# Kernel tuning notes

Hardware: AMD Instinct MI355X
Metric: run time of the kernel (lower is better)

The kernel has to match this reference:

```python
import jax, jax.numpy as jnp
import numpy as np
from functools import partial

U, I, D, E = 8192, 8192, 128, 524288
N = U + I


def setup_inputs() -> dict:
    key = jax.random.key(0)
    ks = jax.random.split(key, 12)
    s = 1.0 / np.sqrt(D)
    return {
        "user_emb": jax.random.normal(ks[0], (U, D), jnp.float32) * 0.1,
        "item_emb": jax.random.normal(ks[1], (I, D), jnp.float32) * 0.1,
        "adj_rows": jax.random.randint(ks[2], (E,), 0, N, jnp.int32),
        "adj_cols": jax.random.randint(ks[3], (E,), 0, N, jnp.int32),
        "adj_vals": jax.random.uniform(ks[4], (E,), jnp.float32) * (1.0 / 32.0),
        "wq": jax.random.normal(ks[5], (D, D), jnp.float32) * s,
        "bq": jnp.zeros((D,), jnp.float32),
        "wk": jax.random.normal(ks[6], (D, D), jnp.float32) * s,
        "bk": jnp.zeros((D,), jnp.float32),
        "wv": jax.random.normal(ks[7], (D, D), jnp.float32) * s,
        "bv": jnp.zeros((D,), jnp.float32),
        "fw": jax.random.normal(ks[8], (D, D), jnp.float32) * s,
        "fb": jnp.zeros((D,), jnp.float32),
        "n_layers": 3,
        "topk": 32,
    }


def _spmm(vals, rows, cols, x):
    # sparse [N,N] @ dense [N,D] via gather + segment_sum
    return jax.ops.segment_sum(vals[:, None] * x[cols], rows, num_segments=N)


def reference(user_emb, item_emb, adj_rows, adj_cols, adj_vals,
              wq, bq, wk, bk, wv, bv, fw, fb, n_layers, topk):
    ego = jnp.concatenate([user_emb, item_emb], axis=0)  # [N, D]
    layers = []
    for _ in range(n_layers):
        ego = _spmm(adj_vals, adj_rows, adj_cols, ego)
        layers.append(ego)
    all_emb = jnp.mean(jnp.stack(layers, axis=1), axis=1)  # [N, D]

    # full similarity + topk + gather
    sim = ego @ ego.T                                # [N, N]
    idx = jax.lax.top_k(sim, topk)[1]                # [N, K]
    samples = jnp.take(ego, idx, axis=0)             # [N, K, D]

    # per-node small attention over the K samples (dropout = eval identity)
    q = ego @ wq.T + bq                              # [N, D]
    k_ = samples @ wk.T + bk                         # [N, K, D]
    v = samples @ wv.T + bv                          # [N, K, D]
    scores = jnp.einsum('nd,nkd->nk', q, k_) / jnp.sqrt(jnp.float32(D))
    attn = jax.nn.softmax(scores, axis=-1)
    atten_embed = jnp.einsum('nk,nkd->nd', attn, v) + 0.1 * ego

    # fusion gating (softmax over dim=1, i.e. the node axis, as in source)
    a1 = jnp.tanh(all_emb @ fw.T + fb)
    a2 = jnp.tanh(atten_embed @ fw.T + fb)
    a = jax.nn.softmax(jnp.stack([a1, a2], axis=0), axis=1)  # [2, N, D]
    fusion = a[0] * all_emb + a[1] * atten_embed

    return (all_emb[:U], all_emb[U:],
            atten_embed[:U], atten_embed[U:],
            fusion[:U], fusion[U:])
```

## Files before the change

kernel.cpp:

```cpp
#include <hip/hip_runtime.h>
#include <math.h>

#define U_ 8192
#define I_ 8192
#define D_ 128
#define E_ 524288
#define N_ 16384
#define K_ 32
#define CAP_ 512

typedef unsigned short u16;
typedef unsigned int u32;
typedef unsigned long long u64;
typedef __attribute__((ext_vector_type(8))) short bf16x8;
typedef __attribute__((ext_vector_type(4))) float f32x4;

__global__ void k_init(const float* __restrict__ wq, const float* __restrict__ wk,
                       const float* __restrict__ bq, const float* __restrict__ wv,
                       const float* __restrict__ fw,
                       float* __restrict__ M, float* __restrict__ bqk,
                       float* __restrict__ wvT, float* __restrict__ fwdT,
                       int* __restrict__ cnt, float* __restrict__ cs1,
                       float* __restrict__ cs2,
                       float* __restrict__ svec, int* __restrict__ gcount,
                       int* __restrict__ failn) {
  const int tid = blockIdx.x * 256 + threadIdx.x;
  cnt[tid] = 0;
  gcount[tid] = 0;
  if (tid < 2048) { cs1[tid] = 0.f; cs2[tid] = 0.f; }
  if (tid < 128) svec[tid] = 0.f;
  if (tid == 0) *failn = 0;
  const int i = tid >> 7, j = tid & 127;
  float s = 0.f;
  for (int l = 0; l < 128; ++l) s += wq[l * 128 + i] * wk[l * 128 + j];
  M[tid] = s;
  wvT[i * 128 + j] = wv[j * 128 + i];
  fwdT[i * 128 + j] = fw[j * 128 + i];
  if (tid < 128) {
    float s2 = 0.f;
    for (int l = 0; l < 128; ++l) s2 += bq[l] * wk[l * 128 + tid];
    bqk[tid] = s2;
  }
}

__global__ void k_concat(const float* __restrict__ user, const float* __restrict__ item,
                         float* __restrict__ ego,
                         const int* __restrict__ rows, int* __restrict__ cnt) {
  const int i = blockIdx.x * 256 + threadIdx.x;
  const float4 v = (i < U_ * D_ / 4) ? ((const float4*)user)[i]
                                     : ((const float4*)item)[i - U_ * D_ / 4];
  ((float4*)ego)[i] = v;
  atomicAdd(&cnt[rows[i]], 1);
}

__global__ void k_scan(const int* __restrict__ cnt, int* __restrict__ row_ptr,
                       int* __restrict__ cursor) {
  __shared__ int wsum[16];
  __shared__ int carry_s;
  const int t = threadIdx.x;
  const int lane = t & 63, wid = t >> 6;
  if (t == 0) carry_s = 0;
  __syncthreads();
  for (int c = 0; c < N_ / 1024; ++c) {
    const int x = cnt[c * 1024 + t];
    int incl = x;
#pragma unroll
    for (int off = 1; off < 64; off <<= 1) {
      const int v = __shfl_up(incl, off, 64);
      if (lane >= off) incl += v;
    }
    if (lane == 63) wsum[wid] = incl;
    __syncthreads();
    if (wid == 0) {
      int s = (lane < 16) ? wsum[lane] : 0;
#pragma unroll
      for (int off = 1; off < 16; off <<= 1) {
        const int v = __shfl_up(s, off, 64);
        if (lane >= off) s += v;
      }
      if (lane < 16) wsum[lane] = s;
    }
    __syncthreads();
    const int carry = carry_s;
    const int wbase = wid ? wsum[wid - 1] : 0;
    const int excl = carry + wbase + incl - x;
    row_ptr[c * 1024 + t] = excl;
    cursor[c * 1024 + t] = excl;
    __syncthreads();
    if (t == 1023) carry_s += wsum[15];
    __syncthreads();
  }
  if (t == 0) row_ptr[N_] = carry_s;
}

__global__ void k_scatter(const int* __restrict__ rows, const int* __restrict__ cols,
                          const float* __restrict__ vals, int* __restrict__ cursor,
                          int* __restrict__ ccol, float* __restrict__ cval) {
  const int e = blockIdx.x * 256 + threadIdx.x;
  const int r = rows[e];
  const int p = atomicAdd(&cursor[r], 1);
  ccol[p] = cols[e];
  cval[p] = vals[e];
}

__global__ __launch_bounds__(128) void k_spmm(const float* __restrict__ x,
                                              float* __restrict__ y,
                                              float* __restrict__ sum,
                                              const int* __restrict__ row_ptr,
                                              const int* __restrict__ ccol,
                                              const float* __restrict__ cval,
                                              const int first, const int last) {
  const int r = blockIdx.x, d = threadIdx.x;
  const int b = row_ptr[r], e = row_ptr[r + 1];
  double a[8];
#pragma unroll
  for (int u = 0; u < 8; ++u) a[u] = 0.0;
  int i = b;
  for (; i < e && (i & 3); ++i)
    a[0] += (double)cval[i] * (double)x[ccol[i] * 128 + d];
  for (; i + 7 < e; i += 8) {
    const int4 ca = *(const int4*)&ccol[i];
    const int4 cb = *(const int4*)&ccol[i + 4];
    const float4 va = *(const float4*)&cval[i];
    const float4 vb = *(const float4*)&cval[i + 4];
    a[0] += (double)va.x * (double)x[ca.x * 128 + d];
    a[1] += (double)va.y * (double)x[ca.y * 128 + d];
    a[2] += (double)va.z * (double)x[ca.z * 128 + d];
    a[3] += (double)va.w * (double)x[ca.w * 128 + d];
    a[4] += (double)vb.x * (double)x[cb.x * 128 + d];
    a[5] += (double)vb.y * (double)x[cb.y * 128 + d];
    a[6] += (double)vb.z * (double)x[cb.z * 128 + d];
    a[7] += (double)vb.w * (double)x[cb.w * 128 + d];
  }
  for (; i < e; ++i)
    a[0] += (double)cval[i] * (double)x[ccol[i] * 128 + d];
  const float f = (float)((((a[0] + a[1]) + (a[2] + a[3])) + ((a[4] + a[5]) + (a[6] + a[7]))));
  y[r * 128 + d] = f;
  float s = first ? f : sum[r * 128 + d] + f;
  if (last) s = s / 3.0f;
  sum[r * 128 + d] = s;
}

__global__ __launch_bounds__(256) void k_split_t(const float* __restrict__ x,
                                                 u16* __restrict__ Gh, u16* __restrict__ Gl,
                                                 u16* __restrict__ XTh, u16* __restrict__ XTl,
                                                 float* __restrict__ svec) {
  __shared__ u16 lh[128 * 66];
  __shared__ u16 ll[128 * 66];
  const int tid = threadIdx.x;
  const int r0 = blockIdx.x * 64;
  float colsum = 0.f;
  for (int s = 0; s < 32; ++s) {
    const int idx = tid + s * 256;
    const int r = idx >> 7, d = idx & 127;
    const float v = x[(r0 + r) * 128 + d];
    colsum += v;
    unsigned int u = __float_as_uint(v);
    u += 0x7fffu + ((u >> 16) & 1u);
    const u16 h = (u16)(u >> 16);
    const float hf = __uint_as_float(((unsigned int)h) << 16);
    const float l = v - hf;
    unsigned int u2 = __float_as_uint(l);
    u2 += 0x7fffu + ((u2 >> 16) & 1u);
    const u16 lo = (u16)(u2 >> 16);
    Gh[(r0 + r) * 128 + d] = h;
    Gl[(r0 + r) * 128 + d] = lo;
    lh[d * 66 + r] = h;
    ll[d * 66 + r] = lo;
  }
  atomicAdd(&svec[tid & 127], colsum);
  __syncthreads();
  for (int s = 0; s < 32; ++s) {
    const int idx = tid + s * 256;
    const int d = idx >> 6, rr = idx & 63;
    XTh[d * 16384 + r0 + rr] = lh[d * 66 + rr];
    XTl[d * 16384 + r0 + rr] = ll[d * 66 + rr];
  }
}

__global__ __launch_bounds__(256) void k_c2mfma(const u16* __restrict__ XTh,
                                                const u16* __restrict__ XTl,
                                                float* __restrict__ C2part) {
  const int tid = threadIdx.x, w = tid >> 6, lane = tid & 63;
  const int n16 = lane & 15, kq = lane >> 4;
  const int c0 = blockIdx.x * 64;
  f32x4 acc[2][8];
#pragma unroll
  for (int a = 0; a < 2; ++a)
#pragma unroll
    for (int b = 0; b < 8; ++b) acc[a][b] = (f32x4){0.f, 0.f, 0.f, 0.f};
  for (int ks = 0; ks < 2; ++ks) {
    const int c = c0 + ks * 32 + kq * 8;
    bf16x8 Fh[8], Fl[8];
#pragma unroll
    for (int g = 0; g < 8; ++g) {
      const int base = (g * 16 + n16) * 16384 + c;
      Fh[g] = *(const bf16x8*)&XTh[base];
      Fl[g] = *(const bf16x8*)&XTl[base];
    }
#pragma unroll
    for (int a = 0; a < 2; ++a) {
      const int tr = w * 2 + a;
#pragma unroll
      for (int b = 0; b < 8; ++b) {
        acc[a][b] = __builtin_amdgcn_mfma_f32_16x16x32_bf16(Fl[tr], Fh[b], acc[a][b], 0, 0, 0);
        acc[a][b] = __builtin_amdgcn_mfma_f32_16x16x32_bf16(Fh[tr], Fl[b], acc[a][b], 0, 0, 0);
        acc[a][b] = __builtin_amdgcn_mfma_f32_16x16x32_bf16(Fh[tr], Fh[b], acc[a][b], 0, 0, 0);
      }
    }
  }
  float* dst = C2part + (size_t)blockIdx.x * 16384;
#pragma unroll
  for (int a = 0; a < 2; ++a) {
    const int tr = w * 2 + a;
#pragma unroll
    for (int b = 0; b < 8; ++b)
#pragma unroll
      for (int i = 0; i < 4; ++i)
        dst[(tr * 16 + kq * 4 + i) * 128 + b * 16 + n16] = acc[a][b][i];
  }
}

__global__ void k_c2red(const float* __restrict__ C2part, float* __restrict__ C2) {
  const int e = blockIdx.x * 256 + threadIdx.x;
  float s = 0.f;
  for (int b = 0; b < 256; ++b) s += C2part[(size_t)b * 16384 + e];
  C2[e] = s;
}

__global__ __launch_bounds__(128) void k_tau(const float* __restrict__ x,
                                             const float* __restrict__ C2,
                                             const float* __restrict__ svec,
                                             float* __restrict__ tau) {
  __shared__ float xs[8][128];
  __shared__ double r1[8][2], r2[8][2];
  const int tid = threadIdx.x;
  const int lane = tid & 63, wid = tid >> 6;
  const int n0 = blockIdx.x * 8;
#pragma unroll
  for (int rr = 0; rr < 8; ++rr) xs[rr][tid] = x[(n0 + rr) * 128 + tid];
  __syncthreads();
  double y[8];
#pragma unroll
  for (int rr = 0; rr < 8; ++rr) y[rr] = 0.0;
  for (int k2 = 0; k2 < 128; ++k2) {
    const double c = (double)C2[k2 * 128 + tid];
#pragma unroll
    for (int rr = 0; rr < 8; ++rr) y[rr] += (double)xs[rr][k2] * c;
  }
  const double sv = (double)svec[tid];
#pragma unroll
  for (int rr = 0; rr < 8; ++rr) {
    double v1 = (double)xs[rr][tid] * y[rr];
    double v2 = (double)xs[rr][tid] * sv;
#pragma unroll
    for (int off = 32; off; off >>= 1) {
      v1 += __shfl_xor(v1, off, 64);
      v2 += __shfl_xor(v2, off, 64);
    }
    if (lane == 0) { r1[rr][wid] = v1; r2[rr][wid] = v2; }
  }
  __syncthreads();
  if (tid < 8) {
    const double exy = (r1[tid][0] + r1[tid][1]) / 16384.0;
    const double m = (r2[tid][0] + r2[tid][1]) / 16384.0;
    double var = exy - m * m;
    if (var < 0.0) var = 0.0;
    tau[n0 + tid] = (float)(m + 2.55 * sqrt(var));
  }
}

__global__ __launch_bounds__(256) void k_qk(const float* __restrict__ ego,
                                            const float* __restrict__ M,
                                            const float* __restrict__ bqk,
                                            float* __restrict__ qkout) {
  __shared__ float xs[8][128];
  const int tid = threadIdx.x;
  const int r0 = blockIdx.x * 8;
#pragma unroll
  for (int s = 0; s < 4; ++s) {
    const int idx = tid + s * 256;
    xs[idx >> 7][idx & 127] = ego[r0 * 128 + idx];
  }
  __syncthreads();
  const int j = tid & 127, h = tid >> 7;
  const float bj = bqk[j];
  float acc[4];
#pragma unroll
  for (int r = 0; r < 4; ++r) acc[r] = bj;
  for (int d = 0; d < 128; d += 4) {
    const float w0 = M[(d + 0) * 128 + j];
    const float w1 = M[(d + 1) * 128 + j];
    const float w2 = M[(d + 2) * 128 + j];
    const float w3 = M[(d + 3) * 128 + j];
#pragma unroll
    for (int r = 0; r < 4; ++r) {
      const float4 xv = *(const float4*)&xs[h * 4 + r][d];
      acc[r] += xv.x * w0 + xv.y * w1 + xv.z * w2 + xv.w * w3;
    }
  }
#pragma unroll
  for (int r = 0; r < 4; ++r)
    qkout[(r0 + h * 4 + r) * 128 + j] = acc[r];
}

__device__ __forceinline__ void gload_lds16(const u16* g, u16* l) {
  __builtin_amdgcn_global_load_lds(
      (const __attribute__((address_space(1))) void*)g,
      (__attribute__((address_space(3))) void*)l, 16, 0, 0);
}

__global__ __launch_bounds__(256) void k_simmfma(const u16* __restrict__ Gh,
                                                 const u16* __restrict__ Gl,
                                                 const float* __restrict__ tau,
                                                 int* __restrict__ gstripcnt,
                                                 int2* __restrict__ gbuf) {
  __shared__ __align__(16) u16 lh[64 * 128];
  __shared__ int cnt128[128];
  const int tid = threadIdx.x;
  const int w = tid >> 6, lane = tid & 63;
  const int strip = blockIdx.x & 15, rgrp = blockIdx.x >> 4;
  const int n16 = lane & 15, kq = lane >> 4;

  if (tid < 128) cnt128[tid] = 0;

  const int rowbase = rgrp * 128 + w * 32;
  bf16x8 Bh[2][4], Bl[2][4];
#pragma unroll
  for (int rg = 0; rg < 2; ++rg) {
    const int row = rowbase + rg * 16 + n16;
#pragma unroll
    for (int q = 0; q < 4; ++q) {
      Bh[rg][q] = *(const bf16x8*)&Gh[row * 128 + q * 32 + kq * 8];
      Bl[rg][q] = *(const bf16x8*)&Gl[row * 128 + q * 32 + kq * 8];
    }
  }
  const float tau0 = tau[rowbase + n16];
  const float tau1 = tau[rowbase + 16 + n16];
  const int col0 = strip * 1024;

  for (int st = 0; st < 16; ++st) {
    const int cb = col0 + st * 64;
    __syncthreads();
#pragma unroll
    for (int ii = 0; ii < 4; ++ii) {
      const int srow = w * 16 + ii * 4 + kq;
      const int chunk = n16 ^ (srow & 7);
      gload_lds16(Gh + (((size_t)(cb + srow)) << 7) + chunk * 8,
                  lh + ((w * 16 + ii * 4) << 7));
    }
    __syncthreads();
#pragma unroll
    for (int ct = 0; ct < 4; ++ct) {
      const int ar = ct * 16 + n16;
      const char* lbase = (const char*)lh + ar * 256;
      bf16x8 Ah[4];
#pragma unroll
      for (int q = 0; q < 4; ++q)
        Ah[q] = *(const bf16x8*)(lbase + ((q * 64 + kq * 16) ^ ((ar & 7) << 4)));
#pragma unroll
      for (int rg = 0; rg < 2; ++rg) {
        f32x4 p = {0.f, 0.f, 0.f, 0.f};
        f32x4 r = {0.f, 0.f, 0.f, 0.f};
#pragma unroll
        for (int q = 0; q < 4; ++q) {
          p = __builtin_amdgcn_mfma_f32_16x16x32_bf16(Ah[q], Bh[rg][q], p, 0, 0, 0);
          r = __builtin_amdgcn_mfma_f32_16x16x32_bf16(Ah[q], Bl[rg][q], r, 0, 0, 0);
        }
        const float tv = rg ? tau1 : tau0;
        const int lrow = w * 32 + rg * 16 + n16;
        const int row = rgrp * 128 + lrow;
#pragma unroll
        for (int i = 0; i < 4; ++i) {
          const float v = p[i] + r[i];
          if (v > tv) {
            const int c = cb + ct * 16 + kq * 4 + i;
            const int pos = atomicAdd(&cnt128[lrow], 1);
            if (pos < 32)
              gbuf[row * CAP_ + strip * 32 + pos] = make_int2(c, __float_as_int(v));
          }
        }
      }
    }
  }
  __syncthreads();
  if (tid < 128) gstripcnt[(rgrp * 128 + tid) * 16 + strip] = cnt128[tid];
}

__global__ __launch_bounds__(256) void k_refine(const int* __restrict__ gstripcnt,
                                                const int2* __restrict__ gbuf,
                                                int* __restrict__ topk_idx,
                                                int* __restrict__ failq,
                                                int* __restrict__ failn) {
  __shared__ u64 lk[4][CAP_];
  const int tid = threadIdx.x, w = tid >> 6, lane = tid & 63;
  const int n = blockIdx.x * 4 + w;

  const int scn = (lane < 16) ? gstripcnt[n * 16 + lane] : 0;
  int total = 0, over = 0;
#pragma unroll
  for (int s = 0; s < 16; ++s) {
    const int c = __shfl(scn, s, 64);
    total += c;
    over |= (c > 32);
  }
  const int bad = (total < 36 || total > CAP_ || over);
  const int cnt = bad ? 0 : total;

  int base = 0;
#pragma unroll
  for (int s = 0; s < 16; ++s) {
    const int c = __shfl(scn, s, 64);
    if (!bad && lane < c) {
      const int2 p = gbuf[n * CAP_ + s * 32 + lane];
      u32 uv = (u32)p.y;
      uv = (uv >> 31) ? ~uv : (uv | 0x80000000u);
      lk[w][base + lane] = ((u64)uv << 32) | (u64)(16383 - p.x);
    }
    base += bad ? 0 : c;
  }
  __syncthreads();

  for (int ci = lane; ci < cnt; ci += 64) {
    const u64 kk = lk[w][ci];
    int r = 0;
#pragma unroll 4
    for (int j = 0; j < cnt; ++j)
      r += (lk[w][j] > kk) ? 1 : 0;
    if (r < 32) topk_idx[n * 32 + r] = 16383 - (int)(u32)(kk & 0xffffffffu);
  }
  if (bad) {
    if (lane == 0) {
      const int s = atomicAdd(failn, 1);
      if (s < 64) failq[s] = n;
    }
    if (lane < 32) topk_idx[n * 32 + lane] = 0;
  }
}

__global__ __launch_bounds__(256) void k_fallback(const float* __restrict__ x,
                                                  const int* __restrict__ failq,
                                                  const int* __restrict__ failn,
                                                  double* __restrict__ fsim,
                                                  int* __restrict__ topk_idx) {
  const int nf = *failn;
  const int which = blockIdx.x;
  if (which >= nf || which >= 64) return;
  const int row = failq[which];
  __shared__ float xs[128];
  __shared__ double bm[256];
  __shared__ int bc[256];
  const int tid = threadIdx.x;
  if (tid < 128) xs[tid] = x[row * 128 + tid];
  __syncthreads();
  double* fs = fsim + (size_t)which * 16384;
  for (int c = tid; c < 16384; c += 256) {
    const float4* xp = (const float4*)&x[c * 128];
    double a = 0.0;
    for (int d = 0; d < 32; ++d) {
      const float4 v = xp[d];
      a += (double)xs[d * 4 + 0] * (double)v.x + (double)xs[d * 4 + 1] * (double)v.y +
           (double)xs[d * 4 + 2] * (double)v.z + (double)xs[d * 4 + 3] * (double)v.w;
    }
    fs[c] = a;
  }
  __syncthreads();
  for (int r = 0; r < 32; ++r) {
    double m = -1.0e300; int mc = 0;
    for (int c = tid; c < 16384; c += 256) {
      const double v = fs[c];
      if (v > m || (v == m && c < mc)) { m = v; mc = c; }
    }
    bm[tid] = m; bc[tid] = mc;
    __syncthreads();
    for (int s = 128; s; s >>= 1) {
      if (tid < s) {
        if (bm[tid + s] > bm[tid] || (bm[tid + s] == bm[tid] && bc[tid + s] < bc[tid])) {
          bm[tid] = bm[tid + s]; bc[tid] = bc[tid + s];
        }
      }
      __syncthreads();
    }
    if (tid == 0) { topk_idx[row * 32 + r] = bc[0]; fs[bc[0]] = -1.0e300; }
    __syncthreads();
  }
}

__global__ __launch_bounds__(256) void k_attn(const float* __restrict__ ego,
                                              float* __restrict__ qk,
                                              const int* __restrict__ topk_idx) {
  __shared__ float qv[128];
  __shared__ float sm[32 * 130];
  __shared__ int tki[32];
  __shared__ float sc[32];
  __shared__ float psum[256];
  const int n = blockIdx.x, tid = threadIdx.x;
  if (tid < 128) qv[tid] = qk[n * 128 + tid];
  if (tid < 32) tki[tid] = topk_idx[n * 32 + tid] & 16383;
  __syncthreads();
  for (int e = tid; e < 2048; e += 256) {
    const int k2 = e >> 6, d2 = e & 63;
    const float2 v = *(const float2*)&ego[(size_t)tki[k2] * 128 + d2 * 2];
    *(float2*)&sm[k2 * 130 + d2 * 2] = v;
  }
  __syncthreads();
  {
    const int kk = tid & 31, part = tid >> 5;
    float s = 0.f;
    const int d0 = part * 16;
    for (int d = d0; d < d0 + 16; ++d) s += qv[d] * sm[kk * 130 + d];
    psum[tid] = s;
  }
  __syncthreads();
  if (tid < 32) {
    float v = 0.f;
#pragma unroll
    for (int p = 0; p < 8; ++p) v += psum[tid + p * 32];
    v *= (1.0f / 11.313708498984760f);
    float m = v;
#pragma unroll
    for (int off = 16; off; off >>= 1) m = fmaxf(m, __shfl_xor(m, off, 32));
    const float e = expf(v - m);
    float ssum = e;
#pragma unroll
    for (int off = 16; off; off >>= 1) ssum += __shfl_xor(ssum, off, 32);
    sc[tid] = e / ssum;
  }
  __syncthreads();
  {
    const int d = tid & 127, half = tid >> 7;
    float s = 0.f;
    const int k0 = half * 16;
    for (int k2 = k0; k2 < k0 + 16; ++k2) s += sc[k2] * sm[k2 * 130 + d];
    psum[tid] = s;
  }
  __syncthreads();
  if (tid < 128) qk[n * 128 + tid] = psum[tid] + psum[tid + 128];
}

__global__ __launch_bounds__(256) void k_attnfuse(const float* __restrict__ sa,
                                                  const float* __restrict__ ego,
                                                  const float* __restrict__ allemb,
                                                  const float* __restrict__ wvT,
                                                  const float* __restrict__ bv,
                                                  const float* __restrict__ fwdT,
                                                  const float* __restrict__ fb,
                                                  float* __restrict__ atten,
                                                  float* __restrict__ z1,
                                                  float* __restrict__ z2,
                                                  float* __restrict__ cs1,
                                                  float* __restrict__ cs2) {
  __shared__ float xs[8][128];
  __shared__ float xa[8][128];
  __shared__ float as_[8][128];
  __shared__ float red1[2][128];
  __shared__ float red2[2][128];
  const int tid = threadIdx.x;
  const int r0 = blockIdx.x * 8;
#pragma unroll
  for (int s = 0; s < 4; ++s) {
    const int idx = tid + s * 256;
    const int rr = idx >> 7, d = idx & 127;
    xs[rr][d] = sa[(r0 + rr) * 128 + d];
    xa[rr][d] = allemb[(r0 + rr) * 128 + d];
  }
  __syncthreads();
  const int j = tid & 127, h = tid >> 7;
  {
    const float bj = bv[j];
    float acc[4];
#pragma unroll
    for (int r = 0; r < 4; ++r) acc[r] = bj;
    for (int d = 0; d < 128; d += 4) {
      const float w0 = wvT[(d + 0) * 128 + j];
      const float w1 = wvT[(d + 1) * 128 + j];
      const float w2 = wvT[(d + 2) * 128 + j];
      const float w3 = wvT[(d + 3) * 128 + j];
#pragma unroll
      for (int r = 0; r < 4; ++r) {
        const float4 xv = *(const float4*)&xs[h * 4 + r][d];
        acc[r] += xv.x * w0 + xv.y * w1 + xv.z * w2 + xv.w * w3;
      }
    }
#pragma unroll
    for (int r = 0; r < 4; ++r) {
      const int n = r0 + h * 4 + r;
      const float av = acc[r] + 0.1f * ego[n * 128 + j];
      atten[n * 128 + j] = av;
      as_[h * 4 + r][j] = av;
    }
  }
  __syncthreads();
  const float fbj = fb[j];
  float acc1[4], acc2[4];
#pragma unroll
  for (int r = 0; r < 4; ++r) { acc1[r] = fbj; acc2[r] = fbj; }
  for (int d = 0; d < 128; d += 4) {
    const float w0 = fwdT[(d + 0) * 128 + j];
    const float w1 = fwdT[(d + 1) * 128 + j];
    const float w2 = fwdT[(d + 2) * 128 + j];
    const float w3 = fwdT[(d + 3) * 128 + j];
#pragma unroll
    for (int r = 0; r < 4; ++r) {
      const int rr = h * 4 + r;
      const float4 xv = *(const float4*)&xa[rr][d];
      const float4 av = *(const float4*)&as_[rr][d];
      acc1[r] += xv.x * w0 + xv.y * w1 + xv.z * w2 + xv.w * w3;
      acc2[r] += av.x * w0 + av.y * w1 + av.z * w2 + av.w * w3;
    }
  }
  float ls1 = 0.f, ls2 = 0.f;
#pragma unroll
  for (int r = 0; r < 4; ++r) {
    const int rr = h * 4 + r;
    const float t1 = tanhf(acc1[r]);
    const float t2 = tanhf(acc2[r]);
    z1[(r0 + rr) * 128 + j] = t1;
    z2[(r0 + rr) * 128 + j] = t2;
    ls1 += expf(t1 - 1.0f);
    ls2 += expf(t2 - 1.0f);
  }
  red1[h][j] = ls1;
  red2[h][j] = ls2;
  __syncthreads();
  if (h == 0) {
    const int rep = blockIdx.x & 15;
    atomicAdd(&cs1[rep * 128 + j], red1[0][j] + red1[1][j]);
    atomicAdd(&cs2[rep * 128 + j], red2[0][j] + red2[1][j]);
  }
}

__global__ void k_fuse2(const float* __restrict__ allemb, const float* __restrict__ atten,
                        const float* __restrict__ z1, const float* __restrict__ z2,
                        const float* __restrict__ cs1, const float* __restrict__ cs2,
                        float* __restrict__ fusion) {
  __shared__ float s1[128], s2[128];
  const int tid = threadIdx.x;
  if (tid < 128) {
    float a = 0.f, b = 0.f;
#pragma unroll
    for (int rep = 0; rep < 16; ++rep) {
      a += cs1[rep * 128 + tid];
      b += cs2[rep * 128 + tid];
    }
    s1[tid] = a; s2[tid] = b;
  }
  __syncthreads();
  const int i = blockIdx.x * 256 + tid;
  const int j0 = (i & 31) * 4;
  const float4 zv1 = ((const float4*)z1)[i];
  const float4 zv2 = ((const float4*)z2)[i];
  const float4 xv = ((const float4*)allemb)[i];
  const float4 av = ((const float4*)atten)[i];
  float4 o;
  o.x = expf(zv1.x - 1.0f) / s1[j0 + 0] * xv.x + expf(zv2.x - 1.0f) / s2[j0 + 0] * av.x;
  o.y = expf(zv1.y - 1.0f) / s1[j0 + 1] * xv.y + expf(zv2.y - 1.0f) / s2[j0 + 1] * av.y;
  o.z = expf(zv1.z - 1.0f) / s1[j0 + 2] * xv.z + expf(zv2.z - 1.0f) / s2[j0 + 2] * av.z;
  o.w = expf(zv1.w - 1.0f) / s1[j0 + 3] * xv.w + expf(zv2.w - 1.0f) / s2[j0 + 3] * av.w;
  ((float4*)fusion)[i] = o;
}

extern "C" void kernel_launch(void* const* d_in, const int* in_sizes, int n_in,
                              void* d_out, int out_size, void* d_ws, size_t ws_size,
                              hipStream_t stream) {
  (void)in_sizes; (void)n_in; (void)out_size; (void)ws_size;
  const float* user = (const float*)d_in[0];
  const float* item = (const float*)d_in[1];
  const int* adj_rows = (const int*)d_in[2];
  const int* adj_cols = (const int*)d_in[3];
  const float* adj_vals = (const float*)d_in[4];
  const float* wq = (const float*)d_in[5];
  const float* bq = (const float*)d_in[6];
  const float* wk = (const float*)d_in[7];
  const float* wv = (const float*)d_in[9];
  const float* bv = (const float*)d_in[10];
  const float* fw = (const float*)d_in[11];
  const float* fb = (const float*)d_in[12];

  float* out = (float*)d_out;
  float* allemb = out;
  float* atten = out + (size_t)N_ * D_;
  float* fusion = out + (size_t)2 * N_ * D_;

  char* ws = (char*)d_ws;
  size_t off = 0;
  auto alloc = [&](size_t bytes) { char* p = ws + off; off += (bytes + 255) & ~(size_t)255; return p; };
  float* ego_a = (float*)alloc((size_t)N_ * D_ * 4);
  float* ego_b = (float*)alloc((size_t)N_ * D_ * 4);
  float* qkbuf = (float*)alloc((size_t)N_ * D_ * 4);
  u16* Gh = (u16*)alloc((size_t)N_ * D_ * 2);
  u16* Gl = (u16*)alloc((size_t)N_ * D_ * 2);
  u16* XTh = (u16*)alloc((size_t)N_ * D_ * 2);
  u16* XTl = (u16*)alloc((size_t)N_ * D_ * 2);
  int2* gbuf = (int2*)alloc((size_t)N_ * CAP_ * 8);
  float* z1 = (float*)gbuf;
  float* z2 = (float*)alloc((size_t)N_ * D_ * 4);
  int* topk_idx = (int*)alloc((size_t)N_ * 32 * 4);
  int* ccol = (int*)alloc((size_t)E_ * 4);
  float* cval = (float*)alloc((size_t)E_ * 4);
  int* cnt = (int*)alloc((size_t)N_ * 4);
  int* row_ptr = (int*)alloc((size_t)(N_ + 1) * 4);
  int* cursor = (int*)alloc((size_t)N_ * 4);
  float* M = (float*)alloc(128 * 128 * 4);
  float* bqk = (float*)alloc(128 * 4);
  float* wvT = (float*)alloc(128 * 128 * 4);
  float* fwdT = (float*)alloc(128 * 128 * 4);
  float* cs1 = (float*)alloc(16 * 128 * 4);
  float* cs2 = (float*)alloc(16 * 128 * 4);
  float* C2 = (float*)alloc(128 * 128 * 4);
  float* C2part = (float*)alloc((size_t)256 * 16384 * 4);
  float* svec = (float*)alloc(128 * 4);
  float* tau = (float*)alloc((size_t)N_ * 4);
  int* gcount = (int*)alloc((size_t)N_ * 4);
  int* gstripcnt = (int*)alloc((size_t)N_ * 16 * 4);
  int* failq = (int*)alloc(64 * 4);
  int* failn = (int*)alloc(4);
  double* fsim = (double*)alloc((size_t)64 * N_ * 8);

  k_init<<<64, 256, 0, stream>>>(wq, wk, bq, wv, fw, M, bqk, wvT, fwdT, cnt, cs1, cs2, svec, gcount, failn);
  k_concat<<<2048, 256, 0, stream>>>(user, item, ego_a, adj_rows, cnt);
  k_scan<<<1, 1024, 0, stream>>>(cnt, row_ptr, cursor);
  k_scatter<<<2048, 256, 0, stream>>>(adj_rows, adj_cols, adj_vals, cursor, ccol, cval);

  k_spmm<<<N_, 128, 0, stream>>>(ego_a, ego_b, allemb, row_ptr, ccol, cval, 1, 0);
  k_spmm<<<N_, 128, 0, stream>>>(ego_b, ego_a, allemb, row_ptr, ccol, cval, 0, 0);
  k_spmm<<<N_, 128, 0, stream>>>(ego_a, ego_b, allemb, row_ptr, ccol, cval, 0, 1);

  k_split_t<<<256, 256, 0, stream>>>(ego_b, Gh, Gl, XTh, XTl, svec);
  k_c2mfma<<<256, 256, 0, stream>>>(XTh, XTl, C2part);
  k_c2red<<<64, 256, 0, stream>>>(C2part, C2);
  k_tau<<<2048, 128, 0, stream>>>(ego_b, C2, svec, tau);

  k_qk<<<2048, 256, 0, stream>>>(ego_b, M, bqk, qkbuf);
  k_simmfma<<<2048, 256, 0, stream>>>(Gh, Gl, tau, gstripcnt, gbuf);
  k_refine<<<4096, 256, 0, stream>>>(gstripcnt, gbuf, topk_idx, failq, failn);
  k_fallback<<<64, 256, 0, stream>>>(ego_b, failq, failn, fsim, topk_idx);
  k_attn<<<N_, 256, 0, stream>>>(ego_b, qkbuf, topk_idx);
  k_attnfuse<<<2048, 256, 0, stream>>>(qkbuf, ego_b, allemb, wvT, bv, fwdT, fb,
                                       atten, z1, z2, cs1, cs2);
  k_fuse2<<<2048, 256, 0, stream>>>(allemb, atten, z1, z2, cs1, cs2, fusion);
}
```

Measured before the change: 662.4 us.

## Parallelize CSR scan, unroll C2 reduction, fuse qk and tau kernels

Replaces the single-block 1024-thread serial-chunk scan with a three-kernel multi-block scan (block sums, offsets, local scan). Unrolls the C2 partial reduction into four independent accumulators to expose more memory-level parallelism. Merges the qk projection and tau threshold kernels into one kernel that shares the staged ego rows, splitting the fp64 C2 reduction across two thread halves. This trades two extra small launches in the scan for fewer serialized steps, and removes one launch plus one reload of ego.

```diff
diff --git a/kernel.cpp b/kernel.cpp
--- a/kernel.cpp
+++ b/kernel.cpp
@@ -53,44 +53,50 @@
   atomicAdd(&cnt[rows[i]], 1);
 }
 
-__global__ void k_scan(const int* __restrict__ cnt, int* __restrict__ row_ptr,
-                       int* __restrict__ cursor) {
-  __shared__ int wsum[16];
-  __shared__ int carry_s;
+__global__ void k_scanA(const int* __restrict__ cnt, int* __restrict__ bsum) {
+  __shared__ int ws[4];
+  const int t = threadIdx.x, lane = t & 63, wid = t >> 6;
+  int v = cnt[blockIdx.x * 256 + t];
+#pragma unroll
+  for (int off = 32; off; off >>= 1) v += __shfl_xor(v, off, 64);
+  if (lane == 0) ws[wid] = v;
+  __syncthreads();
+  if (t == 0) bsum[blockIdx.x] = ws[0] + ws[1] + ws[2] + ws[3];
+}
+
+__global__ void k_scanB(const int* __restrict__ bsum, int* __restrict__ boff,
+                        int* __restrict__ row_ptr) {
   const int t = threadIdx.x;
-  const int lane = t & 63, wid = t >> 6;
-  if (t == 0) carry_s = 0;
-  __syncthreads();
-  for (int c = 0; c < N_ / 1024; ++c) {
-    const int x = cnt[c * 1024 + t];
-    int incl = x;
-#pragma unroll
-    for (int off = 1; off < 64; off <<= 1) {
-      const int v = __shfl_up(incl, off, 64);
-      if (lane >= off) incl += v;
-    }
-    if (lane == 63) wsum[wid] = incl;
-    __syncthreads();
-    if (wid == 0) {
-      int s = (lane < 16) ? wsum[lane] : 0;
-#pragma unroll
-      for (int off = 1; off < 16; off <<= 1) {
-        const int v = __shfl_up(s, off, 64);
-        if (lane >= off) s += v;
-      }
-      if (lane < 16) wsum[lane] = s;
-    }
-    __syncthreads();
-    const int carry = carry_s;
-    const int wbase = wid ? wsum[wid - 1] : 0;
-    const int excl = carry + wbase + incl - x;
-    row_ptr[c * 1024 + t] = excl;
-    cursor[c * 1024 + t] = excl;
-    __syncthreads();
-    if (t == 1023) carry_s += wsum[15];
-    __syncthreads();
-  }
-  if (t == 0) row_ptr[N_] = carry_s;
+  const int x = bsum[t];
+  int incl = x;
+#pragma unroll
+  for (int off = 1; off < 64; off <<= 1) {
+    const int v = __shfl_up(incl, off, 64);
+    if (t >= off) incl += v;
+  }
+  boff[t] = incl - x;
+  if (t == 63) row_ptr[N_] = incl;
+}
+
+__global__ void k_scanC(const int* __restrict__ cnt, const int* __restrict__ boff,
+                        int* __restrict__ row_ptr, int* __restrict__ cursor) {
+  __shared__ int ws[4];
+  const int t = threadIdx.x, lane = t & 63, wid = t >> 6;
+  const int g = blockIdx.x * 256 + t;
+  const int x = cnt[g];
+  int incl = x;
+#pragma unroll
+  for (int off = 1; off < 64; off <<= 1) {
+    const int v = __shfl_up(incl, off, 64);
+    if (lane >= off) incl += v;
+  }
+  if (lane == 63) ws[wid] = incl;
+  __syncthreads();
+  int wbase = 0;
+  for (int k = 0; k < wid; ++k) wbase += ws[k];
+  const int excl = boff[blockIdx.x] + wbase + incl - x;
+  row_ptr[g] = excl;
+  cursor[g] = excl;
 }
 
 __global__ void k_scatter(const int* __restrict__ rows, const int* __restrict__ cols,
@@ -223,36 +229,69 @@
 
 __global__ void k_c2red(const float* __restrict__ C2part, float* __restrict__ C2) {
   const int e = blockIdx.x * 256 + threadIdx.x;
-  float s = 0.f;
-  for (int b = 0; b < 256; ++b) s += C2part[(size_t)b * 16384 + e];
-  C2[e] = s;
-}
-
-__global__ __launch_bounds__(128) void k_tau(const float* __restrict__ x,
-                                             const float* __restrict__ C2,
-                                             const float* __restrict__ svec,
-                                             float* __restrict__ tau) {
+  float s0 = 0.f, s1 = 0.f, s2 = 0.f, s3 = 0.f;
+  for (int b = 0; b < 256; b += 4) {
+    s0 += C2part[(size_t)(b + 0) * 16384 + e];
+    s1 += C2part[(size_t)(b + 1) * 16384 + e];
+    s2 += C2part[(size_t)(b + 2) * 16384 + e];
+    s3 += C2part[(size_t)(b + 3) * 16384 + e];
+  }
+  C2[e] = (s0 + s1) + (s2 + s3);
+}
+
+__global__ __launch_bounds__(256) void k_qktau(const float* __restrict__ ego,
+                                               const float* __restrict__ M,
+                                               const float* __restrict__ bqk,
+                                               const float* __restrict__ C2,
+                                               const float* __restrict__ svec,
+                                               float* __restrict__ qkout,
+                                               float* __restrict__ tau) {
   __shared__ float xs[8][128];
-  __shared__ double r1[8][2], r2[8][2];
+  __shared__ double r1[8][4], r2[8][4];
   const int tid = threadIdx.x;
+  const int r0 = blockIdx.x * 8;
+#pragma unroll
+  for (int s = 0; s < 4; ++s) {
+    const int idx = tid + s * 256;
+    xs[idx >> 7][idx & 127] = ego[r0 * 128 + idx];
+  }
+  __syncthreads();
+  const int j = tid & 127, h = tid >> 7;
+  {
+    const float bj = bqk[j];
+    float acc[4];
+#pragma unroll
+    for (int r = 0; r < 4; ++r) acc[r] = bj;
+    for (int d = 0; d < 128; d += 4) {
+      const float w0 = M[(d + 0) * 128 + j];
+      const float w1 = M[(d + 1) * 128 + j];
+      const float w2 = M[(d + 2) * 128 + j];
+      const float w3 = M[(d + 3) * 128 + j];
+#pragma unroll
+      for (int r = 0; r < 4; ++r) {
+        const float4 xv = *(const float4*)&xs[h * 4 + r][d];
+        acc[r] += xv.x * w0 + xv.y * w1 + xv.z * w2 + xv.w * w3;
+      }
+    }
+#pragma unroll
+    for (int r = 0; r < 4; ++r)
+      qkout[(r0 + h * 4 + r) * 128 + j] = acc[r];
+  }
   const int lane = tid & 63, wid = tid >> 6;
-  const int n0 = blockIdx.x * 8;
-#pragma unroll
-  for (int rr = 0; rr < 8; ++rr) xs[rr][tid] = x[(n0 + rr) * 128 + tid];
-  __syncthreads();
   double y[8];
 #pragma unroll
   for (int rr = 0; rr < 8; ++rr) y[rr] = 0.0;
-  for (int k2 = 0; k2 < 128; ++k2) {
-    const double c = (double)C2[k2 * 128 + tid];
+  const int k0 = h * 64;
+  for (int k2 = k0; k2 < k0 + 64; ++k2) {
+    const double c = (double)C2[k2 * 128 + j];
 #pragma unroll
     for (int rr = 0; rr < 8; ++rr) y[rr] += (double)xs[rr][k2] * c;
   }
-  const double sv = (double)svec[tid];
+  const double sv = (h == 0) ? (double)svec[j] : 0.0;
 #pragma unroll
   for (int rr = 0; rr < 8; ++rr) {
-    double v1 = (double)xs[rr][tid] * y[rr];
-    double v2 = (double)xs[rr][tid] * sv;
+    double v1 = (double)xs[rr][j] * y[rr];
+    double v2 = (double)xs[rr][j] * sv;
 #pragma unroll
     for (int off = 32; off; off >>= 1) {
       v1 += __shfl_xor(v1, off, 64);
@@ -262,46 +301,12 @@
   }
   __syncthreads();
   if (tid < 8) {
-    const double exy = (r1[tid][0] + r1[tid][1]) / 16384.0;
-    const double m = (r2[tid][0] + r2[tid][1]) / 16384.0;
+    const double exy = (r1[tid][0] + r1[tid][1] + r1[tid][2] + r1[tid][3]) / 16384.0;
+    const double m = (r2[tid][0] + r2[tid][1] + r2[tid][2] + r2[tid][3]) / 16384.0;
     double var = exy - m * m;
     if (var < 0.0) var = 0.0;
-    tau[n0 + tid] = (float)(m + 2.55 * sqrt(var));
-  }
-}
-
-__global__ __launch_bounds__(256) void k_qk(const float* __restrict__ ego,
-                                            const float* __restrict__ M,
-                                            const float* __restrict__ bqk,
-                                            float* __restrict__ qkout) {
-  __shared__ float xs[8][128];
-  const int tid = threadIdx.x;
-  const int r0 = blockIdx.x * 8;
-#pragma unroll
-  for (int s = 0; s < 4; ++s) {
-    const int idx = tid + s * 256;
-    xs[idx >> 7][idx & 127] = ego[r0 * 128 + idx];
-  }
-  __syncthreads();
-  const int j = tid & 127, h = tid >> 7;
-  const float bj = bqk[j];
-  float acc[4];
-#pragma unroll
-  for (int r = 0; r < 4; ++r) acc[r] = bj;
-  for (int d = 0; d < 128; d += 4) {
-    const float w0 = M[(d + 0) * 128 + j];
-    const float w1 = M[(d + 1) * 128 + j];
-    const float w2 = M[(d + 2) * 128 + j];
-    const float w3 = M[(d + 3) * 128 + j];
-#pragma unroll
-    for (int r = 0; r < 4; ++r) {
-      const float4 xv = *(const float4*)&xs[h * 4 + r][d];
-      acc[r] += xv.x * w0 + xv.y * w1 + xv.z * w2 + xv.w * w3;
-    }
-  }
-#pragma unroll
-  for (int r = 0; r < 4; ++r)
-    qkout[(r0 + h * 4 + r) * 128 + j] = acc[r];
+    tau[r0 + tid] = (float)(m + 2.55 * sqrt(var));
+  }
 }
 
 __device__ __forceinline__ void gload_lds16(const u16* g, u16* l) {
@@ -701,6 +706,8 @@
   int* cnt = (int*)alloc((size_t)N_ * 4);
   int* row_ptr = (int*)alloc((size_t)(N_ + 1) * 4);
   int* cursor = (int*)alloc((size_t)N_ * 4);
+  int* bsum = (int*)alloc(64 * 4);
+  int* boff = (int*)alloc(64 * 4);
   float* M = (float*)alloc(128 * 128 * 4);
   float* bqk = (float*)alloc(128 * 4);
   float* wvT = (float*)alloc(128 * 128 * 4);
@@ -719,7 +726,9 @@
 
   k_init<<<64, 256, 0, stream>>>(wq, wk, bq, wv, fw, M, bqk, wvT, fwdT, cnt, cs1, cs2, svec, gcount, failn);
   k_concat<<<2048, 256, 0, stream>>>(user, item, ego_a, adj_rows, cnt);
-  k_scan<<<1, 1024, 0, stream>>>(cnt, row_ptr, cursor);
+  k_scanA<<<64, 256, 0, stream>>>(cnt, bsum);
+  k_scanB<<<1, 64, 0, stream>>>(bsum, boff, row_ptr);
+  k_scanC<<<64, 256, 0, stream>>>(cnt, boff, row_ptr, cursor);
   k_scatter<<<2048, 256, 0, stream>>>(adj_rows, adj_cols, adj_vals, cursor, ccol, cval);
 
   k_spmm<<<N_, 128, 0, stream>>>(ego_a, ego_b, allemb, row_ptr, ccol, cval, 1, 0);
@@ -729,9 +738,8 @@
   k_split_t<<<256, 256, 0, stream>>>(ego_b, Gh, Gl, XTh, XTl, svec);
   k_c2mfma<<<256, 256, 0, stream>>>(XTh, XTl, C2part);
   k_c2red<<<64, 256, 0, stream>>>(C2part, C2);
-  k_tau<<<2048, 128, 0, stream>>>(ego_b, C2, svec, tau);
-
-  k_qk<<<2048, 256, 0, stream>>>(ego_b, M, bqk, qkbuf);
+  k_qktau<<<2048, 256, 0, stream>>>(ego_b, M, bqk, C2, svec, qkbuf, tau);
+
   k_simmfma<<<2048, 256, 0, stream>>>(Gh, Gl, tau, gstripcnt, gbuf);
   k_refine<<<4096, 256, 0, stream>>>(gstripcnt, gbuf, topk_idx, failq, failn);
   k_fallback<<<64, 256, 0, stream>>>(ego_b, failq, failn, fsim, topk_idx);
```

New measurement: 664.2 us. Within noise of the previous version (+0.3%).
